# Optimization experiments

Hardware: AMD Instinct MI355X
Metric: run time of the kernel (lower is better)

## Reference

```python
import jax, jax.numpy as jnp
import numpy as np

LAMBDA_COORD = 5.0
LAMBDA_NOOBJ = 0.5
NUM_CLASSES = 80


def setup_inputs() -> dict:
    key = jax.random.key(0)
    k1, k2 = jax.random.split(key)
    B, G, C5, T = 64, 80, NUM_CLASSES + 5, 50
    predictions = jax.random.normal(k1, (B, G, G, C5), dtype=jnp.float32)
    t = jax.random.uniform(k2, (B, T, 5), dtype=jnp.float32)  # coords in [0,1)
    # col 0 holds the class id as a float (cast with .long() in the original)
    targets = t.at[..., 0].set(jnp.floor(t[..., 0] * NUM_CLASSES))
    return {"predictions": predictions, "targets": targets}


def reference(predictions, targets):
    B, G, _, C5 = predictions.shape
    T = targets.shape[1]
    nc = C5 - 5

    cls_id = targets[..., 0].astype(jnp.int32)              # (B,T)
    xg = targets[..., 1] * G
    yg = targets[..., 2] * G
    wg = targets[..., 3] * G
    hg = targets[..., 4] * G

    # obj/coord/class path clamps the cell index (int() truncation == floor for >=0)
    gx = jnp.clip(xg.astype(jnp.int32), 0, G - 1)           # (B,T)
    gy = jnp.clip(yg.astype(jnp.int32), 0, G - 1)
    bidx = jnp.broadcast_to(jnp.arange(B)[:, None], (B, T))
    pred = predictions[bidx, gy, gx]                         # (B,T,C5) gather of responsible cells

    sp = jax.nn.softplus
    # BCEWithLogits(z, 1) = softplus(-z), summed over all targets
    obj_loss = sp(-pred[..., 0]).sum()

    x_t = xg - gx.astype(xg.dtype)
    y_t = yg - gy.astype(yg.dtype)
    coord_loss = LAMBDA_COORD * (
        ((jax.nn.sigmoid(pred[..., 1]) - x_t) ** 2).sum()
        + ((jax.nn.sigmoid(pred[..., 2]) - y_t) ** 2).sum()
        + ((pred[..., 3] - wg) ** 2).sum()
        + ((pred[..., 4] - hg) ** 2).sum()
    )

    # BCEWithLogits(z, onehot) summed = sum softplus(z) - z * t
    z = pred[..., 5:]                                        # (B,T,nc)
    onehot = jax.nn.one_hot(cls_id, nc, dtype=z.dtype)
    class_loss = (sp(z) - z * onehot).sum()

    # noobj path uses the UNclamped truncated index (coords in [0,1) so identical here)
    tx = xg.astype(jnp.int32)
    ty = yg.astype(jnp.int32)
    occupied = jnp.zeros((B, G, G), dtype=bool).at[bidx, ty, tx].set(True)
    noobj_loss = LAMBDA_NOOBJ * jnp.where(
        occupied, jnp.float32(0.0), sp(predictions[..., 0])
    ).sum()

    Bf = jnp.float32(B)
    obj_loss = obj_loss / Bf
    noobj_loss = noobj_loss / Bf
    coord_loss = coord_loss / Bf
    class_loss = class_loss / Bf
    total = obj_loss + noobj_loss + coord_loss + class_loss
    return total, obj_loss, noobj_loss, coord_loss, class_loss
```

## Files before the change

kernel.cpp:

```cpp
#include <hip/hip_runtime.h>
#include <math.h>

#define GRID_SZ 80
#define NT      50
#define C5      85
#define BATCH   64
#define TPB     256
#define CELLS   (GRID_SZ*GRID_SZ)
#define BLKS_PER_IMG (CELLS/TPB)
#define NBLK    (BATCH*BLKS_PER_IMG)
#define MAGIC   0x5A17C0DEu

__device__ __forceinline__ float sp(float x) {
    return fmaxf(x, 0.0f) + __logf(1.0f + __expf(-fabsf(x)));
}


__global__ __launch_bounds__(TPB) void fused_kernel(const float* __restrict__ pred,
                                                    const float* __restrict__ tgt,
                                                    unsigned long long* __restrict__ slots,
                                                    float* __restrict__ out) {
    const int tid  = threadIdx.x;
    const int lane = tid & 63;
    const int w    = tid >> 6;
    const int b    = blockIdx.x / BLKS_PER_IMG;
    const int blk  = blockIdx.x % BLKS_PER_IMG;

    const int   ci = blk * TPB + tid;
    const float p0 = pred[((size_t)b * CELLS + ci) * C5];

    __shared__ unsigned s_bits[TPB / 32];
    __shared__ float    s_red[4][4];

    if (tid < TPB / 32) s_bits[tid] = 0u;
    __syncthreads();

    if (tid < NT) {
        const float* tp = tgt + ((size_t)b * NT + tid) * 5;
        const int tx = (int)(tp[1] * GRID_SZ);
        const int ty = (int)(tp[2] * GRID_SZ);
        const int c  = ty * GRID_SZ + tx - blk * TPB;
        if ((unsigned)c < TPB) atomicOr(&s_bits[c >> 5], 1u << (c & 31));
    }

    float obj = 0.f, coord = 0.f, cls = 0.f;
    if (w < 2) {
        const int gt = blockIdx.x * 2 + w;
        const int tb = gt / NT, tt = gt - tb * NT;
        const float* tp = tgt + ((size_t)tb * NT + tt) * 5;
        const float t0 = tp[0], t1 = tp[1], t2 = tp[2], t3 = tp[3], t4 = tp[4];
        const int   cid = (int)t0;
        const float xg = t1 * GRID_SZ, yg = t2 * GRID_SZ;
        const float wg = t3 * GRID_SZ, hg = t4 * GRID_SZ;
        const int gx = min(max((int)xg, 0), GRID_SZ - 1);
        const int gy = min(max((int)yg, 0), GRID_SZ - 1);
        const float xt = xg - (float)gx;
        const float yt = yg - (float)gy;
        const float* pp = pred + (((size_t)tb * GRID_SZ + gy) * GRID_SZ + gx) * C5;

        {
            const float p = pp[lane];
            if (lane == 0)      obj = sp(-p);
            else if (lane == 1) { const float s = 1.f / (1.f + __expf(-p)); const float d = s - xt; coord = d * d; }
            else if (lane == 2) { const float s = 1.f / (1.f + __expf(-p)); const float d = s - yt; coord = d * d; }
            else if (lane == 3) { const float d = p - wg; coord = d * d; }
            else if (lane == 4) { const float d = p - hg; coord = d * d; }
            else                cls = sp(p) - ((lane - 5) == cid ? p : 0.f);
        }
        const int c2 = lane + 64;
        if (c2 < C5) {
            const float p = pp[c2];
            cls += sp(p) - ((c2 - 5) == cid ? p : 0.f);
        }
    }

    __syncthreads();
    const bool occ = (s_bits[tid >> 5] >> (tid & 31)) & 1u;
    float nob = occ ? 0.f : sp(p0);

    #pragma unroll
    for (int off = 32; off; off >>= 1) {
        obj   += __shfl_xor(obj,   off);
        coord += __shfl_xor(coord, off);
        cls   += __shfl_xor(cls,   off);
        nob   += __shfl_xor(nob,   off);
    }
    if (lane == 0) { s_red[w][0] = obj; s_red[w][1] = coord; s_red[w][2] = cls; s_red[w][3] = nob; }
    __syncthreads();
    if (tid < 4) {
        const float v = s_red[0][tid] + s_red[1][tid] + s_red[2][tid] + s_red[3][tid];
        const unsigned u = __float_as_uint(v);
        const unsigned long long pk =
            (unsigned long long)u | ((unsigned long long)(u ^ MAGIC) << 32);
        __hip_atomic_store(&slots[(size_t)blockIdx.x * 4 + tid], pk,
                           __ATOMIC_RELAXED, __HIP_MEMORY_SCOPE_AGENT);
    }

    if (blockIdx.x == 0) {
        float acc = 0.f;
        #pragma unroll
        for (int g = 0; g < 25; g += 8) {
            const int n = (25 - g) < 8 ? (25 - g) : 8;
            unsigned long long v[8];
            bool ok;
            do {
                ok = true;
                #pragma unroll
                for (int j = 0; j < 8; ++j)
                    if (j < n)
                        v[j] = __hip_atomic_load(&slots[tid + (g + j) * TPB],
                                                 __ATOMIC_RELAXED, __HIP_MEMORY_SCOPE_AGENT);
                #pragma unroll
                for (int j = 0; j < 8; ++j)
                    if (j < n)
                        ok &= ((unsigned)(v[j] >> 32) == (((unsigned)v[j]) ^ MAGIC));
            } while (!ok);
            #pragma unroll
            for (int j = 0; j < 8; ++j)
                if (j < n) acc += __uint_as_float((unsigned)v[j]);
        }

        #pragma unroll
        for (int off = 4; off <= 32; off <<= 1) acc += __shfl_xor(acc, off);

        __shared__ float s_fin[4][4];
        if (lane < 4) s_fin[w][lane] = acc;
        __syncthreads();
        if (tid == 0) {
            float sums[4];
            #pragma unroll
            for (int c = 0; c < 4; ++c)
                sums[c] = s_fin[0][c] + s_fin[1][c] + s_fin[2][c] + s_fin[3][c];
            const float invB  = 1.f / (float)BATCH;
            const float objT   = sums[0] * invB;
            const float coordT = 5.0f * sums[1] * invB;
            const float clsT   = sums[2] * invB;
            const float nobT   = 0.5f * sums[3] * invB;
            out[0] = objT + nobT + coordT + clsT;
            out[1] = objT;
            out[2] = nobT;
            out[3] = coordT;
            out[4] = clsT;
        }
    }
}

extern "C" void kernel_launch(void* const* d_in, const int* in_sizes, int n_in,
                              void* d_out, int out_size, void* d_ws, size_t ws_size,
                              hipStream_t stream) {
    const float* pred = (const float*)d_in[0];
    const float* tgt  = (const float*)d_in[1];
    unsigned long long* slots = (unsigned long long*)d_ws;
    float* out = (float*)d_out;

    fused_kernel<<<NBLK, TPB, 0, stream>>>(pred, tgt, slots, out);
}
```

Measured before the change: 17.94 us.

## Restructure grid to 640 blocks of 320 threads, two cells per thread

Changes the work split from 1600 blocks of 256 threads to 640 blocks of 320 threads. Each thread now handles two noobj cells, and every wavefront handles one target. All waves now do target work, so the idle-wave imbalance goes away and fewer partial slots need reducing. The final reduction in block 0 becomes a single 8-load spin loop instead of four grouped passes. The trade-off is fewer blocks for latency hiding on the strided p0 loads, and a hardcoded bit-offset of 10 words that ties correctness to CPB=640.

After: 15.93 us. -11.2%, faster.

```diff
diff --git a/kernel.cpp b/kernel.cpp
--- a/kernel.cpp
+++ b/kernel.cpp
@@ -5,10 +5,12 @@
 #define NT      50
 #define C5      85
 #define BATCH   64
-#define TPB     256
+#define TPB     320
 #define CELLS   (GRID_SZ*GRID_SZ)
-#define BLKS_PER_IMG (CELLS/TPB)
-#define NBLK    (BATCH*BLKS_PER_IMG)
+#define CPB     640
+#define BPI     10
+#define NBLK    (BATCH*BPI)
+#define NSLOT   (NBLK*4)
 #define MAGIC   0x5A17C0DEu
 
 __device__ __forceinline__ float sp(float x) {
@@ -23,29 +25,30 @@
     const int tid  = threadIdx.x;
     const int lane = tid & 63;
     const int w    = tid >> 6;
-    const int b    = blockIdx.x / BLKS_PER_IMG;
-    const int blk  = blockIdx.x % BLKS_PER_IMG;
+    const int b    = blockIdx.x / BPI;
+    const int blk  = blockIdx.x % BPI;
 
-    const int   ci = blk * TPB + tid;
-    const float p0 = pred[((size_t)b * CELLS + ci) * C5];
+    const size_t cellbase = (size_t)b * CELLS + blk * CPB;
+    const float p0a = pred[(cellbase + tid)       * C5];
+    const float p0b = pred[(cellbase + tid + TPB) * C5];
 
-    __shared__ unsigned s_bits[TPB / 32];
-    __shared__ float    s_red[4][4];
+    __shared__ unsigned s_bits[CPB / 32];
+    __shared__ float    s_red[5][4];
 
-    if (tid < TPB / 32) s_bits[tid] = 0u;
+    if (tid < CPB / 32) s_bits[tid] = 0u;
     __syncthreads();
 
     if (tid < NT) {
         const float* tp = tgt + ((size_t)b * NT + tid) * 5;
         const int tx = (int)(tp[1] * GRID_SZ);
         const int ty = (int)(tp[2] * GRID_SZ);
-        const int c  = ty * GRID_SZ + tx - blk * TPB;
-        if ((unsigned)c < TPB) atomicOr(&s_bits[c >> 5], 1u << (c & 31));
+        const int c  = ty * GRID_SZ + tx - blk * CPB;
+        if ((unsigned)c < CPB) atomicOr(&s_bits[c >> 5], 1u << (c & 31));
     }
 
     float obj = 0.f, coord = 0.f, cls = 0.f;
-    if (w < 2) {
-        const int gt = blockIdx.x * 2 + w;
+    {
+        const int gt = blockIdx.x * 5 + w;
         const int tb = gt / NT, tt = gt - tb * NT;
         const float* tp = tgt + ((size_t)tb * NT + tt) * 5;
         const float t0 = tp[0], t1 = tp[1], t2 = tp[2], t3 = tp[3], t4 = tp[4];
@@ -75,8 +78,9 @@
     }
 
     __syncthreads();
-    const bool occ = (s_bits[tid >> 5] >> (tid & 31)) & 1u;
-    float nob = occ ? 0.f : sp(p0);
+    const bool occA = (s_bits[tid >> 5]        >> (tid & 31)) & 1u;
+    const bool occB = (s_bits[(tid >> 5) + 10] >> (tid & 31)) & 1u;
+    float nob = (occA ? 0.f : sp(p0a)) + (occB ? 0.f : sp(p0b));
 
     #pragma unroll
     for (int off = 32; off; off >>= 1) {
@@ -88,7 +92,7 @@
     if (lane == 0) { s_red[w][0] = obj; s_red[w][1] = coord; s_red[w][2] = cls; s_red[w][3] = nob; }
     __syncthreads();
     if (tid < 4) {
-        const float v = s_red[0][tid] + s_red[1][tid] + s_red[2][tid] + s_red[3][tid];
+        const float v = s_red[0][tid] + s_red[1][tid] + s_red[2][tid] + s_red[3][tid] + s_red[4][tid];
         const unsigned u = __float_as_uint(v);
         const unsigned long long pk =
             (unsigned long long)u | ((unsigned long long)(u ^ MAGIC) << 32);
@@ -97,41 +101,34 @@
     }
 
     if (blockIdx.x == 0) {
+        unsigned long long v[8];
+        bool ok;
+        do {
+            ok = true;
+            #pragma unroll
+            for (int j = 0; j < 8; ++j)
+                v[j] = __hip_atomic_load(&slots[tid + j * TPB],
+                                         __ATOMIC_RELAXED, __HIP_MEMORY_SCOPE_AGENT);
+            #pragma unroll
+            for (int j = 0; j < 8; ++j)
+                ok &= ((unsigned)(v[j] >> 32) == (((unsigned)v[j]) ^ MAGIC));
+        } while (!ok);
         float acc = 0.f;
         #pragma unroll
-        for (int g = 0; g < 25; g += 8) {
-            const int n = (25 - g) < 8 ? (25 - g) : 8;
-            unsigned long long v[8];
-            bool ok;
-            do {
-                ok = true;
-                #pragma unroll
-                for (int j = 0; j < 8; ++j)
-                    if (j < n)
-                        v[j] = __hip_atomic_load(&slots[tid + (g + j) * TPB],
-                                                 __ATOMIC_RELAXED, __HIP_MEMORY_SCOPE_AGENT);
-                #pragma unroll
-                for (int j = 0; j < 8; ++j)
-                    if (j < n)
-                        ok &= ((unsigned)(v[j] >> 32) == (((unsigned)v[j]) ^ MAGIC));
-            } while (!ok);
-            #pragma unroll
-            for (int j = 0; j < 8; ++j)
-                if (j < n) acc += __uint_as_float((unsigned)v[j]);
-        }
+        for (int j = 0; j < 8; ++j) acc += __uint_as_float((unsigned)v[j]);
 
         #pragma unroll
         for (int off = 4; off <= 32; off <<= 1) acc += __shfl_xor(acc, off);
 
-        __shared__ float s_fin[4][4];
+        __shared__ float s_fin[5][4];
         if (lane < 4) s_fin[w][lane] = acc;
         __syncthreads();
         if (tid == 0) {
             float sums[4];
             #pragma unroll
             for (int c = 0; c < 4; ++c)
-                sums[c] = s_fin[0][c] + s_fin[1][c] + s_fin[2][c] + s_fin[3][c];
-            const float invB  = 1.f / (float)BATCH;
+                sums[c] = s_fin[0][c] + s_fin[1][c] + s_fin[2][c] + s_fin[3][c] + s_fin[4][c];
+            const float invB   = 1.f / (float)BATCH;
             const float objT   = sums[0] * invB;
             const float coordT = 5.0f * sums[1] * invB;
             const float clsT   = sums[2] * invB;
```
